# Kernel optimization log

Measured on AMD Instinct MI355X. Metric: run time of the kernel, lower is better.

The kernel has to match this reference:

```python
import jax, jax.numpy as jnp
import numpy as np

HEADS = 16
EMBED = 1024
HEAD_DIM = EMBED // HEADS


def setup_inputs() -> dict:
    key = jax.random.key(0)
    ks = jax.random.split(key, 11)
    B, S, E = 4, 2048, EMBED
    s = 1.0 / np.sqrt(E)
    return {
        "query": jax.random.normal(ks[0], (B, S, E), jnp.float32),
        "key": jax.random.normal(ks[1], (B, S, E), jnp.float32),
        "value": jax.random.normal(ks[2], (B, S, E), jnp.float32),
        "Wq": jax.random.normal(ks[3], (E, E), jnp.float32) * s,
        "bq": jax.random.normal(ks[4], (E,), jnp.float32) * s,
        "Wk": jax.random.normal(ks[5], (E, E), jnp.float32) * s,
        "bk": jax.random.normal(ks[6], (E,), jnp.float32) * s,
        "Wv": jax.random.normal(ks[7], (E, E), jnp.float32) * s,
        "bv": jax.random.normal(ks[8], (E,), jnp.float32) * s,
        "Wo": jax.random.normal(ks[9], (E, E), jnp.float32) * s,
        "bo": jax.random.normal(ks[10], (E,), jnp.float32) * s,
    }


def reference(query, key, value, Wq, bq, Wk, bk, Wv, bv, Wo, bo):
    B, Sq, E = query.shape
    Sk = key.shape[1]
    H, D = HEADS, HEAD_DIM
    # linear projections (torch Linear: x @ W.T + b)
    q = (query @ Wq.T + bq).reshape(B, Sq, H, D)
    k = (key @ Wk.T + bk).reshape(B, Sk, H, D)
    v = (value @ Wv.T + bv).reshape(B, Sk, H, D)
    scores = jnp.einsum("bqhd,bkhd->bhqk", q, k) / np.sqrt(D).astype(jnp.float32)
    attn = jax.nn.softmax(scores, axis=-1)
    out = jnp.einsum("bhqk,bkhd->bqhd", attn, v).reshape(B, Sq, E)
    # dropout p=0.0 -> identity
    return out @ Wo.T + bo
```

## Files before the change

kernel.cpp:

```cpp
#include <hip/hip_runtime.h>
#include <hip/hip_bf16.h>
#include <stdint.h>

#define BATCH 4
#define SEQ   2048
#define EMB   1024
#define NHEAD 16
#define HDIM  64

typedef __bf16 bf16x8 __attribute__((ext_vector_type(8)));
typedef float  f32x4  __attribute__((ext_vector_type(4)));
typedef float  f32x16 __attribute__((ext_vector_type(16)));

__global__ __launch_bounds__(256) void cvt_f32_bf16(const float* __restrict__ in,
                                                    __bf16* __restrict__ out, int n4) {
  int i = blockIdx.x * 256 + threadIdx.x;
  if (i >= n4) return;
  float4 v = reinterpret_cast<const float4*>(in)[i];
  union { ushort4 u; __bf16 b[4]; } o;
  o.b[0] = (__bf16)v.x; o.b[1] = (__bf16)v.y;
  o.b[2] = (__bf16)v.z; o.b[3] = (__bf16)v.w;
  reinterpret_cast<ushort4*>(out)[i] = o.u;
}

__device__ __forceinline__ void gload_lds16(const void* g, void* l) {
  __builtin_amdgcn_global_load_lds((const uint32_t __attribute__((address_space(1)))*)g,
                                   (uint32_t __attribute__((address_space(3)))*)l, 16, 0, 0);
}

enum { EPI_BF16 = 0, EPI_F32 = 1, EPI_VT = 2 };

template <int MODE>
__global__ __launch_bounds__(512, 2)
void gemm2(const __bf16* __restrict__ A, const __bf16* __restrict__ Bt,
           const float* __restrict__ bias, void* __restrict__ Cout,
           int M, int N, int K) {
  __shared__ __bf16 As[2][256 * 64];
  __shared__ __bf16 Bs[2][128 * 64];

  const int tid  = threadIdx.x;
  const int wave = tid >> 6, lane = tid & 63;
  const int l4 = lane >> 4, l15 = lane & 15;
  const int row0 = blockIdx.x * 256, col0 = blockIdx.y * 128;
  const int wr = (wave >> 1) * 64, wc = (wave & 1) * 64;

  const int sr = tid >> 3;
  const int scb = ((tid & 7) * 16) ^ ((sr & 7) << 4);
  const char* gA = (const char*)A  + ((size_t)(row0 + sr) * K) * 2 + scb;
  const char* gB = (const char*)Bt + ((size_t)(col0 + sr) * K) * 2 + scb;
  const size_t rstride = (size_t)64 * K * 2;

  f32x4 acc[4][4] = {};

  auto STAGE = [&](int bi, int t) {
    char* lA = (char*)&As[bi][0] + wave * 1024;
    char* lB = (char*)&Bs[bi][0] + wave * 1024;
    const size_t ko = (size_t)t * 128;
#pragma unroll
    for (int c = 0; c < 4; ++c)
      gload_lds16(gA + ko + c * rstride, lA + c * 8192);
#pragma unroll
    for (int c = 0; c < 2; ++c)
      gload_lds16(gB + ko + c * rstride, lB + c * 8192);
  };

  const int NT = K >> 6;
  STAGE(0, 0);
  asm volatile("s_waitcnt vmcnt(0)" ::: "memory");
  __builtin_amdgcn_s_barrier();
  __builtin_amdgcn_sched_barrier(0);

  const int swz = (l15 & 7) << 4;
  int cur = 0;
  for (int t = 0; t < NT; ++t) {
    if (t + 1 < NT) STAGE(cur ^ 1, t + 1);

    const char* la = (const char*)&As[cur][0];
    const char* lb = (const char*)&Bs[cur][0];
    bf16x8 af[4][2], bfv[4][2];
#pragma unroll
    for (int m = 0; m < 4; ++m)
#pragma unroll
      for (int k = 0; k < 2; ++k)
        af[m][k] = *(const bf16x8*)(la + (wr + m * 16 + l15) * 128 + ((k * 64 + l4 * 16) ^ swz));
#pragma unroll
    for (int n = 0; n < 4; ++n)
#pragma unroll
      for (int k = 0; k < 2; ++k)
        bfv[n][k] = *(const bf16x8*)(lb + (wc + n * 16 + l15) * 128 + ((k * 64 + l4 * 16) ^ swz));

    asm volatile("s_waitcnt lgkmcnt(0)" ::: "memory");
    __builtin_amdgcn_sched_barrier(0);
    __builtin_amdgcn_s_setprio(1);
#pragma unroll
    for (int k = 0; k < 2; ++k)
#pragma unroll
      for (int m = 0; m < 4; ++m)
#pragma unroll
        for (int n = 0; n < 4; ++n)
          acc[m][n] = __builtin_amdgcn_mfma_f32_16x16x32_bf16(af[m][k], bfv[n][k], acc[m][n], 0, 0, 0);
    __builtin_amdgcn_s_setprio(0);

    asm volatile("s_waitcnt vmcnt(0)" ::: "memory");
    __builtin_amdgcn_s_barrier();
    __builtin_amdgcn_sched_barrier(0);
    cur ^= 1;
  }

#pragma unroll
  for (int m = 0; m < 4; ++m) {
    const int r = row0 + wr + m * 16 + l4 * 4;
#pragma unroll
    for (int n = 0; n < 4; ++n) {
      const int c  = col0 + wc + n * 16 + l15;
      const float bb = bias[c];
      if (MODE == EPI_F32) {
        float* C = (float*)Cout;
#pragma unroll
        for (int i = 0; i < 4; ++i) C[(size_t)(r + i) * N + c] = acc[m][n][i] + bb;
      } else if (MODE == EPI_BF16) {
        __bf16* C = (__bf16*)Cout;
#pragma unroll
        for (int i = 0; i < 4; ++i) C[(size_t)(r + i) * N + c] = (__bf16)(acc[m][n][i] + bb);
      } else {
        const int b = r >> 11, s = r & (SEQ - 1);
        const int h = c >> 6, d = c & (HDIM - 1);
        union { ushort4 u; __bf16 x[4]; } o;
#pragma unroll
        for (int i = 0; i < 4; ++i) o.x[i] = (__bf16)(acc[m][n][i] + bb);
        *(ushort4*)((__bf16*)Cout + ((size_t)((b * NHEAD + h) * HDIM + d)) * SEQ + s) = o.u;
      }
    }
  }
}

__device__ __forceinline__ f32x16 mfma32(bf16x8 a, bf16x8 b, f32x16 c) {
  return __builtin_amdgcn_mfma_f32_32x32x16_bf16(a, b, c, 0, 0, 0);
}

__global__ __launch_bounds__(512, 2)
void attn_fwd2(const __bf16* __restrict__ Q, const __bf16* __restrict__ Kk,
               const __bf16* __restrict__ Vt, __bf16* __restrict__ O) {
  __shared__ __bf16 Ks[2][64 * 64];
  __shared__ __bf16 Vs[2][64 * 64];

  const int tid = threadIdx.x;
  const int w = tid >> 6, lane = tid & 63;
  const int l31 = lane & 31, hi = lane >> 5;
  const int bh = blockIdx.x, b = bh >> 4, h = bh & 15;
  const int q0 = blockIdx.y * 256 + w * 32;

  bf16x8 qf[4];
  {
    const __bf16* qb = Q + (size_t)(b * SEQ + q0 + l31) * EMB + h * HDIM + hi * 8;
#pragma unroll
    for (int ks = 0; ks < 4; ++ks) {
      bf16x8 t = *(const bf16x8*)(qb + ks * 16);
#pragma unroll
      for (int j = 0; j < 8; ++j) t[j] = (__bf16)((float)t[j] * 0.1803368801111244f);
      qf[ks] = t;
    }
  }

  const int srow = w * 8 + (lane >> 3);
  const int sswz = ((lane & 7) * 16) ^ ((srow & 7) << 4);
  const char* kg = (const char*)(Kk + (size_t)(b * SEQ) * EMB + h * HDIM)
                   + (size_t)srow * (EMB * 2) + sswz;
  const char* vg = (const char*)(Vt + (size_t)((b * NHEAD + h) * HDIM) * SEQ)
                   + (size_t)srow * (SEQ * 2) + sswz;

  auto STAGE = [&](int bi, int t) {
    gload_lds16(kg + (size_t)t * (64 * EMB * 2), (char*)&Ks[bi][0] + w * 1024);
    gload_lds16(vg + (size_t)t * 128,            (char*)&Vs[bi][0] + w * 1024);
  };

  f32x16 oacc0 = {}, oacc1 = {};
  float mx = -1e30f, ls = 0.f;
  const int rswz = (l31 & 7) << 4;

  STAGE(0, 0);
  for (int t = 0; t < 32; ++t) {
    const int bi = t & 1;
    if (t < 31) {
      STAGE(bi ^ 1, t + 1);
      asm volatile("s_waitcnt vmcnt(2)" ::: "memory");
    } else {
      asm volatile("s_waitcnt vmcnt(0)" ::: "memory");
    }
    __builtin_amdgcn_s_barrier();
    __builtin_amdgcn_sched_barrier(0);

    f32x16 sc0 = {}, sc1 = {};
    const char* kb = (const char*)&Ks[bi][0];
#pragma unroll
    for (int ks = 0; ks < 4; ++ks) {
      const int o = (ks * 32 + hi * 16) ^ rswz;
      bf16x8 k0 = *(const bf16x8*)(kb + l31 * 128 + o);
      bf16x8 k1 = *(const bf16x8*)(kb + (l31 + 32) * 128 + o);
      sc0 = mfma32(k0, qf[ks], sc0);
      sc1 = mfma32(k1, qf[ks], sc1);
    }

    float pm = sc0[0];
#pragma unroll
    for (int r = 1; r < 16; ++r) pm = fmaxf(pm, sc0[r]);
#pragma unroll
    for (int r = 0; r < 16; ++r) pm = fmaxf(pm, sc1[r]);
    pm = fmaxf(pm, __shfl_xor(pm, 32));
    const float mn = fmaxf(mx, pm);
    const float corr = exp2f(mx - mn);
    mx = mn;
    float rs = 0.f;
#pragma unroll
    for (int r = 0; r < 16; ++r) { sc0[r] = exp2f(sc0[r] - mn); rs += sc0[r]; }
#pragma unroll
    for (int r = 0; r < 16; ++r) { sc1[r] = exp2f(sc1[r] - mn); rs += sc1[r]; }
    rs += __shfl_xor(rs, 32);
    ls = ls * corr + rs;
#pragma unroll
    for (int r = 0; r < 16; ++r) { oacc0[r] *= corr; oacc1[r] *= corr; }

    union Fu { uint32_t w[4]; bf16x8 v; };
    auto pk = [](float a, float b) -> uint32_t {
      union { __bf16 h[2]; uint32_t u; } z;
      z.h[0] = (__bf16)a; z.h[1] = (__bf16)b; return z.u;
    };
    bf16x8 pa[4];
    {
      uint32_t A0 = pk(sc0[0], sc0[1]),  A1 = pk(sc0[2], sc0[3]);
      uint32_t B0 = pk(sc0[4], sc0[5]),  B1 = pk(sc0[6], sc0[7]);
      uint32_t C0 = pk(sc0[8], sc0[9]),  C1 = pk(sc0[10], sc0[11]);
      uint32_t D0 = pk(sc0[12], sc0[13]), D1 = pk(sc0[14], sc0[15]);
      uint32_t sA0 = __shfl_xor((int)A0, 32), sA1 = __shfl_xor((int)A1, 32);
      uint32_t sB0 = __shfl_xor((int)B0, 32), sB1 = __shfl_xor((int)B1, 32);
      uint32_t sC0 = __shfl_xor((int)C0, 32), sC1 = __shfl_xor((int)C1, 32);
      uint32_t sD0 = __shfl_xor((int)D0, 32), sD1 = __shfl_xor((int)D1, 32);
      Fu f0, f1;
      f0.w[0] = hi ? sB0 : A0;  f0.w[1] = hi ? sB1 : A1;
      f0.w[2] = hi ? B0 : sA0;  f0.w[3] = hi ? B1 : sA1;
      f1.w[0] = hi ? sD0 : C0;  f1.w[1] = hi ? sD1 : C1;
      f1.w[2] = hi ? D0 : sC0;  f1.w[3] = hi ? D1 : sC1;
      pa[0] = f0.v; pa[1] = f1.v;
      uint32_t E0 = pk(sc1[0], sc1[1]),  E1 = pk(sc1[2], sc1[3]);
      uint32_t F0 = pk(sc1[4], sc1[5]),  F1 = pk(sc1[6], sc1[7]);
      uint32_t G0 = pk(sc1[8], sc1[9]),  G1 = pk(sc1[10], sc1[11]);
      uint32_t H0 = pk(sc1[12], sc1[13]), H1 = pk(sc1[14], sc1[15]);
      uint32_t sE0 = __shfl_xor((int)E0, 32), sE1 = __shfl_xor((int)E1, 32);
      uint32_t sF0 = __shfl_xor((int)F0, 32), sF1 = __shfl_xor((int)F1, 32);
      uint32_t sG0 = __shfl_xor((int)G0, 32), sG1 = __shfl_xor((int)G1, 32);
      uint32_t sH0 = __shfl_xor((int)H0, 32), sH1 = __shfl_xor((int)H1, 32);
      Fu f2, f3;
      f2.w[0] = hi ? sF0 : E0;  f2.w[1] = hi ? sF1 : E1;
      f2.w[2] = hi ? F0 : sE0;  f2.w[3] = hi ? F1 : sE1;
      f3.w[0] = hi ? sH0 : G0;  f3.w[1] = hi ? sH1 : G1;
      f3.w[2] = hi ? H0 : sG0;  f3.w[3] = hi ? H1 : sG1;
      pa[2] = f2.v; pa[3] = f3.v;
    }

    const char* vb = (const char*)&Vs[bi][0];
#pragma unroll
    for (int ks = 0; ks < 4; ++ks) {
      const int o = (ks * 32 + hi * 16) ^ rswz;
      bf16x8 v0 = *(const bf16x8*)(vb + l31 * 128 + o);
      bf16x8 v1 = *(const bf16x8*)(vb + (l31 + 32) * 128 + o);
      oacc0 = mfma32(v0, pa[ks], oacc0);
      oacc1 = mfma32(v1, pa[ks], oacc1);
    }

    __builtin_amdgcn_s_barrier();
    __builtin_amdgcn_sched_barrier(0);
  }

  const float inv = 1.f / ls;
  __bf16* ob = O + (size_t)(b * SEQ + q0 + l31) * EMB + h * HDIM;
#pragma unroll
  for (int c = 0; c < 4; ++c) {
    union { ushort4 u; __bf16 x[4]; } o0, o1;
#pragma unroll
    for (int i = 0; i < 4; ++i) {
      o0.x[i] = (__bf16)(oacc0[4 * c + i] * inv);
      o1.x[i] = (__bf16)(oacc1[4 * c + i] * inv);
    }
    *(ushort4*)(ob + 8 * c + 4 * hi)      = o0.u;
    *(ushort4*)(ob + 32 + 8 * c + 4 * hi) = o1.u;
  }
}

extern "C" void kernel_launch(void* const* d_in, const int* in_sizes, int n_in,
                              void* d_out, int out_size, void* d_ws, size_t ws_size,
                              hipStream_t stream) {
  const float* query = (const float*)d_in[0];
  const float* key   = (const float*)d_in[1];
  const float* value = (const float*)d_in[2];
  const float* Wq = (const float*)d_in[3]; const float* bq = (const float*)d_in[4];
  const float* Wk = (const float*)d_in[5]; const float* bk = (const float*)d_in[6];
  const float* Wv = (const float*)d_in[7]; const float* bv = (const float*)d_in[8];
  const float* Wo = (const float*)d_in[9]; const float* bo = (const float*)d_in[10];

  char* ws = (char*)d_ws;
  const size_t MB = 1u << 20;
  __bf16* Xb  = (__bf16*)(ws);
  __bf16* Qb  = (__bf16*)(ws + 16 * MB);
  __bf16* Kb  = (__bf16*)(ws + 32 * MB);
  __bf16* Vt  = (__bf16*)(ws + 48 * MB);
  __bf16* Wqb = (__bf16*)(ws + 64 * MB);
  __bf16* Wkb = (__bf16*)(ws + 66 * MB);
  __bf16* Wvb = (__bf16*)(ws + 68 * MB);
  __bf16* Wob = (__bf16*)(ws + 70 * MB);

  const int NE = BATCH * SEQ * EMB;
  const int NW = EMB * EMB;
  const int M = BATCH * SEQ;

  dim3 blk(256);
  dim3 gg(M / 256, EMB / 128);
  dim3 gblk(512);

  cvt_f32_bf16<<<dim3(NW / 4 / 256), blk, 0, stream>>>(Wq, Wqb, NW / 4);
  cvt_f32_bf16<<<dim3(NW / 4 / 256), blk, 0, stream>>>(Wk, Wkb, NW / 4);
  cvt_f32_bf16<<<dim3(NW / 4 / 256), blk, 0, stream>>>(Wv, Wvb, NW / 4);
  cvt_f32_bf16<<<dim3(NW / 4 / 256), blk, 0, stream>>>(Wo, Wob, NW / 4);

  cvt_f32_bf16<<<dim3(NE / 4 / 256), blk, 0, stream>>>(query, Xb, NE / 4);
  gemm2<EPI_BF16><<<gg, gblk, 0, stream>>>(Xb, Wqb, bq, Qb, M, EMB, EMB);
  cvt_f32_bf16<<<dim3(NE / 4 / 256), blk, 0, stream>>>(key, Xb, NE / 4);
  gemm2<EPI_BF16><<<gg, gblk, 0, stream>>>(Xb, Wkb, bk, Kb, M, EMB, EMB);
  cvt_f32_bf16<<<dim3(NE / 4 / 256), blk, 0, stream>>>(value, Xb, NE / 4);
  gemm2<EPI_VT><<<gg, gblk, 0, stream>>>(Xb, Wvb, bv, Vt, M, EMB, EMB);

  attn_fwd2<<<dim3(BATCH * NHEAD, SEQ / 256), gblk, 0, stream>>>(Qb, Kb, Vt, Xb);

  gemm2<EPI_F32><<<gg, gblk, 0, stream>>>(Xb, Wob, bo, d_out, M, EMB, EMB);
}
```

Baseline: 413.7 us.

## Triple-buffer GEMM LDS staging and use native exp2 in attention softmax

The projection GEMM moves from a double-buffered to a triple-buffered LDS pipeline. Tiles are prefetched two steps ahead, and partial vmcnt waits replace the full drain at the end of each iteration. LDS use rises to about 144KB per block, and the launch_bounds occupancy hint of 2 is dropped, so only one block fits per CU. The attention softmax also switches exp2f to the native hardware exp2, which trades a little accuracy for fewer instructions.

```diff
diff --git a/kernel.cpp b/kernel.cpp
--- a/kernel.cpp
+++ b/kernel.cpp
@@ -11,6 +11,8 @@
 typedef __bf16 bf16x8 __attribute__((ext_vector_type(8)));
 typedef float  f32x4  __attribute__((ext_vector_type(4)));
 typedef float  f32x16 __attribute__((ext_vector_type(16)));
+
+extern "C" __device__ float __ocml_native_exp2_f32(float);
 
 __global__ __launch_bounds__(256) void cvt_f32_bf16(const float* __restrict__ in,
                                                     __bf16* __restrict__ out, int n4) {
@@ -31,12 +33,12 @@
 enum { EPI_BF16 = 0, EPI_F32 = 1, EPI_VT = 2 };
 
 template <int MODE>
-__global__ __launch_bounds__(512, 2)
-void gemm2(const __bf16* __restrict__ A, const __bf16* __restrict__ Bt,
+__global__ __launch_bounds__(512)
+void gemm3(const __bf16* __restrict__ A, const __bf16* __restrict__ Bt,
            const float* __restrict__ bias, void* __restrict__ Cout,
            int M, int N, int K) {
-  __shared__ __bf16 As[2][256 * 64];
-  __shared__ __bf16 Bs[2][128 * 64];
+  __shared__ __bf16 As[3][256 * 64];
+  __shared__ __bf16 Bs[3][128 * 64];
 
   const int tid  = threadIdx.x;
   const int wave = tid >> 6, lane = tid & 63;
@@ -66,14 +68,22 @@
 
   const int NT = K >> 6;
   STAGE(0, 0);
-  asm volatile("s_waitcnt vmcnt(0)" ::: "memory");
-  __builtin_amdgcn_s_barrier();
-  __builtin_amdgcn_sched_barrier(0);
+  STAGE(1, 1);
 
   const int swz = (l15 & 7) << 4;
   int cur = 0;
   for (int t = 0; t < NT; ++t) {
-    if (t + 1 < NT) STAGE(cur ^ 1, t + 1);
+    if (t + 2 < NT) {
+      int nb = cur + 2; if (nb >= 3) nb -= 3;
+      STAGE(nb, t + 2);
+      asm volatile("s_waitcnt vmcnt(12)" ::: "memory");
+    } else if (t + 1 < NT) {
+      asm volatile("s_waitcnt vmcnt(6)" ::: "memory");
+    } else {
+      asm volatile("s_waitcnt vmcnt(0)" ::: "memory");
+    }
+    __builtin_amdgcn_s_barrier();
+    __builtin_amdgcn_sched_barrier(0);
 
     const char* la = (const char*)&As[cur][0];
     const char* lb = (const char*)&Bs[cur][0];
@@ -101,10 +111,9 @@
           acc[m][n] = __builtin_amdgcn_mfma_f32_16x16x32_bf16(af[m][k], bfv[n][k], acc[m][n], 0, 0, 0);
     __builtin_amdgcn_s_setprio(0);
 
-    asm volatile("s_waitcnt vmcnt(0)" ::: "memory");
     __builtin_amdgcn_s_barrier();
     __builtin_amdgcn_sched_barrier(0);
-    cur ^= 1;
+    ++cur; if (cur >= 3) cur = 0;
   }
 
 #pragma unroll
@@ -208,13 +217,13 @@
     for (int r = 0; r < 16; ++r) pm = fmaxf(pm, sc1[r]);
     pm = fmaxf(pm, __shfl_xor(pm, 32));
     const float mn = fmaxf(mx, pm);
-    const float corr = exp2f(mx - mn);
+    const float corr = __ocml_native_exp2_f32(mx - mn);
     mx = mn;
     float rs = 0.f;
 #pragma unroll
-    for (int r = 0; r < 16; ++r) { sc0[r] = exp2f(sc0[r] - mn); rs += sc0[r]; }
-#pragma unroll
-    for (int r = 0; r < 16; ++r) { sc1[r] = exp2f(sc1[r] - mn); rs += sc1[r]; }
+    for (int r = 0; r < 16; ++r) { sc0[r] = __ocml_native_exp2_f32(sc0[r] - mn); rs += sc0[r]; }
+#pragma unroll
+    for (int r = 0; r < 16; ++r) { sc1[r] = __ocml_native_exp2_f32(sc1[r] - mn); rs += sc1[r]; }
     rs += __shfl_xor(rs, 32);
     ls = ls * corr + rs;
 #pragma unroll
@@ -322,13 +331,13 @@
   cvt_f32_bf16<<<dim3(NW / 4 / 256), blk, 0, stream>>>(Wo, Wob, NW / 4);
 
   cvt_f32_bf16<<<dim3(NE / 4 / 256), blk, 0, stream>>>(query, Xb, NE / 4);
-  gemm2<EPI_BF16><<<gg, gblk, 0, stream>>>(Xb, Wqb, bq, Qb, M, EMB, EMB);
+  gemm3<EPI_BF16><<<gg, gblk, 0, stream>>>(Xb, Wqb, bq, Qb, M, EMB, EMB);
   cvt_f32_bf16<<<dim3(NE / 4 / 256), blk, 0, stream>>>(key, Xb, NE / 4);
-  gemm2<EPI_BF16><<<gg, gblk, 0, stream>>>(Xb, Wkb, bk, Kb, M, EMB, EMB);
+  gemm3<EPI_BF16><<<gg, gblk, 0, stream>>>(Xb, Wkb, bk, Kb, M, EMB, EMB);
   cvt_f32_bf16<<<dim3(NE / 4 / 256), blk, 0, stream>>>(value, Xb, NE / 4);
-  gemm2<EPI_VT><<<gg, gblk, 0, stream>>>(Xb, Wvb, bv, Vt, M, EMB, EMB);
+  gemm3<EPI_VT><<<gg, gblk, 0, stream>>>(Xb, Wvb, bv, Vt, M, EMB, EMB);
 
   attn_fwd2<<<dim3(BATCH * NHEAD, SEQ / 256), gblk, 0, stream>>>(Qb, Kb, Vt, Xb);
 
-  gemm2<EPI_F32><<<gg, gblk, 0, stream>>>(Xb, Wob, bo, d_out, M, EMB, EMB);
-}
+  gemm3<EPI_F32><<<gg, gblk, 0, stream>>>(Xb, Wob, bo, d_out, M, EMB, EMB);
+}
```

New measurement: 379.5 us. 1.09x faster.
